# Optimization experiments

Hardware: AMD Instinct MI355X
Metric: run time of the kernel (lower is better)

Reference implementation:

```python
import jax, jax.numpy as jnp
import numpy as np

N_NODES = 20000
N_EDGES = 320000
IN_CH = 256
HID_CH = 256   # 2 * out_channels
OUT_CH = 128


def gcn_conv(x, edge_index, W, b, n_nodes):
    """PyG GCNConv: linear transform, add self-loops, sym-normalized scatter-add."""
    x = x @ W  # [N, C_out]
    loop = jnp.arange(n_nodes, dtype=edge_index.dtype)
    row = jnp.concatenate([edge_index[0], loop])  # source nodes
    col = jnp.concatenate([edge_index[1], loop])  # destination nodes
    deg = jax.ops.segment_sum(jnp.ones_like(col, dtype=x.dtype), col,
                              num_segments=n_nodes)
    deg_inv_sqrt = jnp.where(deg > 0, jax.lax.rsqrt(deg), 0.0)
    norm = deg_inv_sqrt[row] * deg_inv_sqrt[col]  # [E+N]
    msg = x[row] * norm[:, None]                  # gather + scale
    out = jax.ops.segment_sum(msg, col, num_segments=n_nodes)  # scatter-add
    return out + b


def setup_inputs() -> dict:
    key = jax.random.key(0)
    k1, k2, k3, k4, k5 = jax.random.split(key, 5)
    doc_embeds = jax.random.normal(k1, (N_NODES, IN_CH), dtype=jnp.float32)
    edge_index = jax.random.randint(k2, (2, N_EDGES), 0, N_NODES, dtype=jnp.int64)
    # Glorot-style init for GCN weights, zero bias (PyG defaults)
    s1 = 1.0 / np.sqrt(IN_CH)
    s2 = 1.0 / np.sqrt(HID_CH)
    W1 = jax.random.uniform(k3, (IN_CH, HID_CH), jnp.float32, -s1, s1)
    b1 = jnp.zeros((HID_CH,), jnp.float32)
    W2 = jax.random.uniform(k4, (HID_CH, OUT_CH), jnp.float32, -s2, s2)
    b2 = jnp.zeros((OUT_CH,), jnp.float32)
    return {"doc_embeds": doc_embeds, "edge_index": edge_index,
            "W1": W1, "b1": b1, "W2": W2, "b2": b2}


def reference(doc_embeds, edge_index, W1, b1, W2, b2):
    n = doc_embeds.shape[0]
    x = jax.nn.relu(gcn_conv(doc_embeds, edge_index, W1, b1, n))
    x = gcn_conv(x, edge_index, W2, b2, n)
    return x
```

## Files before the change

kernel.cpp:

```cpp
#include <hip/hip_runtime.h>
#include <math.h>

#define N_NODES 20000
#define N_EDGES 320000
#define IN_CH   256
#define HID_CH  256
#define OUT_CH  128
#define CAP     64

typedef __attribute__((ext_vector_type(8))) short short8;
typedef __attribute__((ext_vector_type(8))) unsigned short ushort8;
typedef __attribute__((ext_vector_type(4))) unsigned short ushort4v;
typedef __attribute__((ext_vector_type(4))) float floatx4;
typedef __attribute__((ext_vector_type(2))) float floatx2;
typedef __attribute__((ext_vector_type(4))) _Float16 half4;
typedef __attribute__((ext_vector_type(2))) _Float16 half2v;
typedef __attribute__((ext_vector_type(8))) _Float16 half8;

static __device__ __forceinline__ unsigned short f2bf(float f) {
    unsigned int u = __float_as_uint(f);
    u += 0x7FFFu + ((u >> 16) & 1u);
    return (unsigned short)(u >> 16);
}
static __device__ __forceinline__ float bf2f(unsigned short h) {
    return __uint_as_float(((unsigned int)h) << 16);
}

__global__ __launch_bounds__(256)
void prep_kernel(const float* __restrict__ W1, const float* __restrict__ W2,
                 unsigned short* __restrict__ W1thi, unsigned short* __restrict__ W1tlo,
                 unsigned short* __restrict__ W2thi, unsigned short* __restrict__ W2tlo,
                 const int* __restrict__ row, const int* __restrict__ col,
                 int* __restrict__ deg, unsigned short* __restrict__ srcs) {
    const int g = blockIdx.x * blockDim.x + threadIdx.x;
    const int gsz = gridDim.x * blockDim.x;
    for (int t = g; t < (IN_CH * HID_CH) / 16; t += gsz) {
        int n = t >> 4;
        int kc = (t & 15) * 16;
        ushort8 h0, l0, h1, l1;
#pragma unroll
        for (int j = 0; j < 8; ++j) {
            float x = W1[(size_t)(kc + j) * HID_CH + n];
            h0[j] = f2bf(x); l0[j] = f2bf(x - bf2f(h0[j]));
            float y = W1[(size_t)(kc + 8 + j) * HID_CH + n];
            h1[j] = f2bf(y); l1[j] = f2bf(y - bf2f(h1[j]));
        }
        *(ushort8*)(W1thi + (size_t)n * IN_CH + kc)     = h0;
        *(ushort8*)(W1thi + (size_t)n * IN_CH + kc + 8) = h1;
        *(ushort8*)(W1tlo + (size_t)n * IN_CH + kc)     = l0;
        *(ushort8*)(W1tlo + (size_t)n * IN_CH + kc + 8) = l1;
    }
    for (int t = g; t < (HID_CH * OUT_CH) / 16; t += gsz) {
        int n = t >> 4;
        int kc = (t & 15) * 16;
        ushort8 h0, l0, h1, l1;
#pragma unroll
        for (int j = 0; j < 8; ++j) {
            float x = W2[(size_t)(kc + j) * OUT_CH + n];
            h0[j] = f2bf(x); l0[j] = f2bf(x - bf2f(h0[j]));
            float y = W2[(size_t)(kc + 8 + j) * OUT_CH + n];
            h1[j] = f2bf(y); l1[j] = f2bf(y - bf2f(h1[j]));
        }
        *(ushort8*)(W2thi + (size_t)n * HID_CH + kc)     = h0;
        *(ushort8*)(W2thi + (size_t)n * HID_CH + kc + 8) = h1;
        *(ushort8*)(W2tlo + (size_t)n * HID_CH + kc)     = l0;
        *(ushort8*)(W2tlo + (size_t)n * HID_CH + kc + 8) = l1;
    }
    for (int i = g; i < N_EDGES; i += gsz) {
        int c = col[i];
        int r = row[i];
        int p = atomicAdd(&deg[c], 1);
        srcs[(size_t)c * CAP + p] = (unsigned short)r;
    }
}

#define GK 256
template <int AMODE, int TM>
__global__ __launch_bounds__(256)
void gemm_mfma_kernel(const float* __restrict__ Afp, const _Float16* __restrict__ Ah,
                      const unsigned short* __restrict__ Bthi, const unsigned short* __restrict__ Btlo,
                      const int* __restrict__ deg, _Float16* __restrict__ C, int M, int N) {
    constexpr int MI = TM / 32;
    __shared__ unsigned short As[2][TM][36];
    __shared__ unsigned short Bs[2][128][36];
    const int tid = threadIdx.x;
    const int m0 = blockIdx.y * TM;
    const int n0 = blockIdx.x * 128;
    const int lane = tid & 63;
    const int wave = tid >> 6;
    const int wr = (wave >> 1) * (TM / 2);
    const int wc = (wave & 1) * 64;
    const int lm = lane & 15;
    const int lk = (lane >> 4) * 8;

    floatx4 acc[MI][4];
#pragma unroll
    for (int i = 0; i < MI; ++i)
#pragma unroll
        for (int j = 0; j < 4; ++j) acc[i][j] = (floatx4){0.f, 0.f, 0.f, 0.f};

    for (int k0 = 0; k0 < GK; k0 += 32) {
#pragma unroll
        for (int c = 0; c < TM / 64; ++c) {
            int ch = tid + c * 256;
            int r = ch >> 2;
            int ko = (ch & 3) * 8;
            ushort8 vh = {}, vl = {};
            if (m0 + r < M) {
                float xs[8];
                if (AMODE == 1) {
                    const float* ap = Afp + (size_t)(m0 + r) * GK + k0 + ko;
                    float4 f0 = *(const float4*)ap;
                    float4 f1 = *(const float4*)(ap + 4);
                    xs[0] = f0.x; xs[1] = f0.y; xs[2] = f0.z; xs[3] = f0.w;
                    xs[4] = f1.x; xs[5] = f1.y; xs[6] = f1.z; xs[7] = f1.w;
                } else {
                    half8 hv = *(const half8*)(Ah + (size_t)(m0 + r) * GK + k0 + ko);
#pragma unroll
                    for (int j = 0; j < 8; ++j) xs[j] = (float)hv[j];
                }
#pragma unroll
                for (int j = 0; j < 8; ++j) {
                    vh[j] = f2bf(xs[j]);
                    vl[j] = f2bf(xs[j] - bf2f(vh[j]));
                }
            }
            *(ushort8*)&As[0][r][ko] = vh;
            *(ushort8*)&As[1][r][ko] = vl;
        }
#pragma unroll
        for (int c = 0; c < 2; ++c) {
            int ch = tid + c * 256;
            int r = ch >> 2;
            int ko = (ch & 3) * 8;
            size_t gb = (size_t)(n0 + r) * GK + k0 + ko;
            *(ushort8*)&Bs[0][r][ko] = *(const ushort8*)(Bthi + gb);
            *(ushort8*)&Bs[1][r][ko] = *(const ushort8*)(Btlo + gb);
        }
        __syncthreads();

        short8 ah[MI], al[MI], bh[4], bl[4];
#pragma unroll
        for (int i = 0; i < MI; ++i) {
            ah[i] = *(const short8*)&As[0][wr + i * 16 + lm][lk];
            al[i] = *(const short8*)&As[1][wr + i * 16 + lm][lk];
        }
#pragma unroll
        for (int j = 0; j < 4; ++j) {
            bh[j] = *(const short8*)&Bs[0][wc + j * 16 + lm][lk];
            bl[j] = *(const short8*)&Bs[1][wc + j * 16 + lm][lk];
        }
#pragma unroll
        for (int i = 0; i < MI; ++i)
#pragma unroll
            for (int j = 0; j < 4; ++j) {
                acc[i][j] = __builtin_amdgcn_mfma_f32_16x16x32_bf16(ah[i], bh[j], acc[i][j], 0, 0, 0);
                acc[i][j] = __builtin_amdgcn_mfma_f32_16x16x32_bf16(ah[i], bl[j], acc[i][j], 0, 0, 0);
                acc[i][j] = __builtin_amdgcn_mfma_f32_16x16x32_bf16(al[i], bh[j], acc[i][j], 0, 0, 0);
            }
        __syncthreads();
    }

#pragma unroll
    for (int i = 0; i < MI; ++i) {
#pragma unroll
        for (int r = 0; r < 4; ++r) {
            int rowi = m0 + wr + i * 16 + (lane >> 4) * 4 + r;
            if (rowi < M) {
                float dr = 1.0f / sqrtf((float)(deg[rowi] + 1));
#pragma unroll
                for (int j = 0; j < 4; ++j) {
                    C[(size_t)rowi * N + n0 + wc + j * 16 + lm] = (_Float16)(dr * acc[i][j][r]);
                }
            }
        }
    }
}

template <int C, int NSLICE, int MODE>
__global__ __launch_bounds__(256)
void gather_sliced_kernel(const _Float16* __restrict__ X, const int* __restrict__ deg,
                          const unsigned short* __restrict__ srcs,
                          const float* __restrict__ bias, float* __restrict__ outf,
                          _Float16* __restrict__ outh, int n) {
    constexpr int SW = C / NSLICE;
    static_assert(SW == 32, "slice must be 32 channels");
    const int slice = blockIdx.x % NSLICE;
    const int ngrp  = blockIdx.x / NSLICE;
    const int wave = threadIdx.x >> 6;
    const int lane = threadIdx.x & 63;
    const int g  = lane >> 4;
    const int sl = lane & 15;
    const int node = ngrp * 16 + wave * 4 + g;
    if (node >= n) return;
    const int choff = slice * SW + sl * 2;
    const size_t beg = (size_t)node * CAP;
    const int cnt = deg[node];

    float a0 = 0.f, a1 = 0.f;
    int e = 0;
    for (; e + 4 <= cnt; e += 4) {
        ushort4v s4 = *(const ushort4v*)(srcs + beg + e);
        half2v v0 = *(const half2v*)(X + (size_t)s4.x * C + choff);
        half2v v1 = *(const half2v*)(X + (size_t)s4.y * C + choff);
        half2v v2 = *(const half2v*)(X + (size_t)s4.z * C + choff);
        half2v v3 = *(const half2v*)(X + (size_t)s4.w * C + choff);
        a0 += (float)v0.x + (float)v1.x + (float)v2.x + (float)v3.x;
        a1 += (float)v0.y + (float)v1.y + (float)v2.y + (float)v3.y;
    }
    for (; e < cnt; ++e) {
        int r = srcs[beg + e];
        half2v v = *(const half2v*)(X + (size_t)r * C + choff);
        a0 += (float)v.x; a1 += (float)v.y;
    }

    const float dc = 1.0f / sqrtf((float)(cnt + 1));
    half2v vsh = *(const half2v*)(X + (size_t)node * C + choff);
    float2 bb = *(const float2*)(bias + choff);

    float o0 = dc * (a0 + (float)vsh.x) + bb.x;
    float o1 = dc * (a1 + (float)vsh.y) + bb.y;

    if constexpr (MODE == 1) {
        half2v h;
        h.x = (_Float16)fmaxf(o0, 0.f);
        h.y = (_Float16)fmaxf(o1, 0.f);
        *(half2v*)(outh + (size_t)node * C + choff) = h;
    } else {
        floatx2 o = {o0, o1};
        __builtin_nontemporal_store(o, (floatx2*)(outf + (size_t)node * C + choff));
    }
}

extern "C" void kernel_launch(void* const* d_in, const int* in_sizes, int n_in,
                              void* d_out, int out_size, void* d_ws, size_t ws_size,
                              hipStream_t stream) {
    const float* doc_embeds = (const float*)d_in[0];
    const int*   edge_index = (const int*)d_in[1];
    const float* W1 = (const float*)d_in[2];
    const float* b1 = (const float*)d_in[3];
    const float* W2 = (const float*)d_in[4];
    const float* b2 = (const float*)d_in[5];
    float* out = (float*)d_out;

    const int* row = edge_index;
    const int* col = edge_index + N_EDGES;

    char* ws = (char*)d_ws;
    auto align_up = [](size_t x) { return (x + 255) / 256 * 256; };

    _Float16* X1s = (_Float16*)(ws);
    _Float16* H1  = (_Float16*)(ws + align_up((size_t)N_NODES * HID_CH * 2));
    _Float16* X2s = X1s;
    char* meta = (char*)(ws + 2 * align_up((size_t)N_NODES * HID_CH * 2));
    unsigned short* W1thi = (unsigned short*)(meta); meta += align_up((size_t)IN_CH * HID_CH * 2);
    unsigned short* W1tlo = (unsigned short*)(meta); meta += align_up((size_t)IN_CH * HID_CH * 2);
    unsigned short* W2thi = (unsigned short*)(meta); meta += align_up((size_t)HID_CH * OUT_CH * 2);
    unsigned short* W2tlo = (unsigned short*)(meta); meta += align_up((size_t)HID_CH * OUT_CH * 2);
    int*            deg   = (int*)(meta);            meta += align_up((size_t)N_NODES * 4);
    unsigned short* srcs  = (unsigned short*)(meta);

    hipMemsetAsync(deg, 0, (size_t)N_NODES * 4, stream);
    prep_kernel<<<(N_EDGES + 255) / 256, 256, 0, stream>>>(
        W1, W2, W1thi, W1tlo, W2thi, W2tlo, row, col, deg, srcs);

    {
        dim3 grid(HID_CH / 128, (N_NODES + 63) / 64);
        gemm_mfma_kernel<1, 64><<<grid, 256, 0, stream>>>(
            doc_embeds, nullptr, W1thi, W1tlo, deg, X1s, N_NODES, HID_CH);
    }
    gather_sliced_kernel<HID_CH, 8, 1><<<((N_NODES + 15) / 16) * 8, 256, 0, stream>>>(
        X1s, deg, srcs, b1, nullptr, H1, N_NODES);

    {
        dim3 grid(OUT_CH / 128, (N_NODES + 63) / 64);
        gemm_mfma_kernel<2, 64><<<grid, 256, 0, stream>>>(
            nullptr, H1, W2thi, W2tlo, deg, X2s, N_NODES, OUT_CH);
    }
    gather_sliced_kernel<OUT_CH, 4, 0><<<((N_NODES + 15) / 16) * 4, 256, 0, stream>>>(
        X2s, deg, srcs, b2, out, nullptr, N_NODES);
}
```

Measured before the change: 174.5 us.

## Pre-split GEMM A operands into bf16 hi/lo planes outside the GEMM loop

The fp32 input embeddings are now split into bf16 hi/lo arrays once in the prep kernel, and the first aggregation writes its ReLU output directly as bf16 hi/lo planes instead of fp16. The GEMM then loads its A tiles straight from those planes with no per-tile conversion, so both column blocks of the first GEMM no longer redo the split. The second GEMM switches to a 64-wide N tile, giving two column blocks for more parallelism. The cost is more workspace and extra global traffic to write and re-read the split arrays, and the prep kernel does more work serially ahead of everything else.

```diff
diff --git a/kernel.cpp b/kernel.cpp
--- a/kernel.cpp
+++ b/kernel.cpp
@@ -7,15 +7,15 @@
 #define HID_CH  256
 #define OUT_CH  128
 #define CAP     64
+#define GK      256
 
 typedef __attribute__((ext_vector_type(8))) short short8;
 typedef __attribute__((ext_vector_type(8))) unsigned short ushort8;
 typedef __attribute__((ext_vector_type(4))) unsigned short ushort4v;
+typedef __attribute__((ext_vector_type(2))) unsigned short ushort2v;
 typedef __attribute__((ext_vector_type(4))) float floatx4;
 typedef __attribute__((ext_vector_type(2))) float floatx2;
-typedef __attribute__((ext_vector_type(4))) _Float16 half4;
 typedef __attribute__((ext_vector_type(2))) _Float16 half2v;
-typedef __attribute__((ext_vector_type(8))) _Float16 half8;
 
 static __device__ __forceinline__ unsigned short f2bf(float f) {
     unsigned int u = __float_as_uint(f);
@@ -28,8 +28,10 @@
 
 __global__ __launch_bounds__(256)
 void prep_kernel(const float* __restrict__ W1, const float* __restrict__ W2,
+                 const float* __restrict__ doc,
                  unsigned short* __restrict__ W1thi, unsigned short* __restrict__ W1tlo,
                  unsigned short* __restrict__ W2thi, unsigned short* __restrict__ W2tlo,
+                 unsigned short* __restrict__ Ehi, unsigned short* __restrict__ Elo,
                  const int* __restrict__ row, const int* __restrict__ col,
                  int* __restrict__ deg, unsigned short* __restrict__ srcs) {
     const int g = blockIdx.x * blockDim.x + threadIdx.x;
@@ -66,6 +68,27 @@
         *(ushort8*)(W2tlo + (size_t)n * HID_CH + kc)     = l0;
         *(ushort8*)(W2tlo + (size_t)n * HID_CH + kc + 8) = l1;
     }
+    for (int t = g; t < (N_NODES * IN_CH) / 16; t += gsz) {
+        int node = t >> 4;
+        int kc = (t & 15) * 16;
+        const float* ap = doc + (size_t)node * IN_CH + kc;
+        float4 f0 = *(const float4*)(ap);
+        float4 f1 = *(const float4*)(ap + 4);
+        float4 f2 = *(const float4*)(ap + 8);
+        float4 f3 = *(const float4*)(ap + 12);
+        float xs[16] = {f0.x, f0.y, f0.z, f0.w, f1.x, f1.y, f1.z, f1.w,
+                        f2.x, f2.y, f2.z, f2.w, f3.x, f3.y, f3.z, f3.w};
+        ushort8 h0, l0, h1, l1;
+#pragma unroll
+        for (int j = 0; j < 8; ++j) {
+            h0[j] = f2bf(xs[j]);     l0[j] = f2bf(xs[j] - bf2f(h0[j]));
+            h1[j] = f2bf(xs[8 + j]); l1[j] = f2bf(xs[8 + j] - bf2f(h1[j]));
+        }
+        *(ushort8*)(Ehi + (size_t)node * IN_CH + kc)     = h0;
+        *(ushort8*)(Ehi + (size_t)node * IN_CH + kc + 8) = h1;
+        *(ushort8*)(Elo + (size_t)node * IN_CH + kc)     = l0;
+        *(ushort8*)(Elo + (size_t)node * IN_CH + kc + 8) = l1;
+    }
     for (int i = g; i < N_EDGES; i += gsz) {
         int c = col[i];
         int r = row[i];
@@ -74,64 +97,48 @@
     }
 }
 
-#define GK 256
-template <int AMODE, int TM>
+template <int TN>
 __global__ __launch_bounds__(256)
-void gemm_mfma_kernel(const float* __restrict__ Afp, const _Float16* __restrict__ Ah,
+void gemm_mfma_kernel(const unsigned short* __restrict__ Ahi, const unsigned short* __restrict__ Alo,
                       const unsigned short* __restrict__ Bthi, const unsigned short* __restrict__ Btlo,
                       const int* __restrict__ deg, _Float16* __restrict__ C, int M, int N) {
-    constexpr int MI = TM / 32;
-    __shared__ unsigned short As[2][TM][36];
-    __shared__ unsigned short Bs[2][128][36];
+    constexpr int NJ = TN / 32;
+    __shared__ unsigned short As[2][64][36];
+    __shared__ unsigned short Bs[2][TN][36];
     const int tid = threadIdx.x;
-    const int m0 = blockIdx.y * TM;
-    const int n0 = blockIdx.x * 128;
+    const int m0 = blockIdx.y * 64;
+    const int n0 = blockIdx.x * TN;
     const int lane = tid & 63;
     const int wave = tid >> 6;
-    const int wr = (wave >> 1) * (TM / 2);
-    const int wc = (wave & 1) * 64;
+    const int wr = (wave >> 1) * 32;
+    const int wc = (wave & 1) * (TN / 2);
     const int lm = lane & 15;
     const int lk = (lane >> 4) * 8;
 
-    floatx4 acc[MI][4];
-#pragma unroll
-    for (int i = 0; i < MI; ++i)
-#pragma unroll
-        for (int j = 0; j < 4; ++j) acc[i][j] = (floatx4){0.f, 0.f, 0.f, 0.f};
+    floatx4 acc[2][NJ];
+#pragma unroll
+    for (int i = 0; i < 2; ++i)
+#pragma unroll
+        for (int j = 0; j < NJ; ++j) acc[i][j] = (floatx4){0.f, 0.f, 0.f, 0.f};
+
+    const int ar  = tid >> 2;
+    const int ako = (tid & 3) * 8;
 
     for (int k0 = 0; k0 < GK; k0 += 32) {
-#pragma unroll
-        for (int c = 0; c < TM / 64; ++c) {
+        {
+            ushort8 vh = {}, vl = {};
+            if (m0 + ar < M) {
+                size_t ga = (size_t)(m0 + ar) * GK + k0 + ako;
+                vh = *(const ushort8*)(Ahi + ga);
+                vl = *(const ushort8*)(Alo + ga);
+            }
+            *(ushort8*)&As[0][ar][ako] = vh;
+            *(ushort8*)&As[1][ar][ako] = vl;
+        }
+#pragma unroll
+        for (int c = 0; c < TN / 64; ++c) {
             int ch = tid + c * 256;
-            int r = ch >> 2;
-            int ko = (ch & 3) * 8;
-            ushort8 vh = {}, vl = {};
-            if (m0 + r < M) {
-                float xs[8];
-                if (AMODE == 1) {
-                    const float* ap = Afp + (size_t)(m0 + r) * GK + k0 + ko;
-                    float4 f0 = *(const float4*)ap;
-                    float4 f1 = *(const float4*)(ap + 4);
-                    xs[0] = f0.x; xs[1] = f0.y; xs[2] = f0.z; xs[3] = f0.w;
-                    xs[4] = f1.x; xs[5] = f1.y; xs[6] = f1.z; xs[7] = f1.w;
-                } else {
-                    half8 hv = *(const half8*)(Ah + (size_t)(m0 + r) * GK + k0 + ko);
-#pragma unroll
-                    for (int j = 0; j < 8; ++j) xs[j] = (float)hv[j];
-                }
-#pragma unroll
-                for (int j = 0; j < 8; ++j) {
-                    vh[j] = f2bf(xs[j]);
-                    vl[j] = f2bf(xs[j] - bf2f(vh[j]));
-                }
-            }
-            *(ushort8*)&As[0][r][ko] = vh;
-            *(ushort8*)&As[1][r][ko] = vl;
-        }
-#pragma unroll
-        for (int c = 0; c < 2; ++c) {
-            int ch = tid + c * 256;
-            int r = ch >> 2;
+            int r  = ch >> 2;
             int ko = (ch & 3) * 8;
             size_t gb = (size_t)(n0 + r) * GK + k0 + ko;
             *(ushort8*)&Bs[0][r][ko] = *(const ushort8*)(Bthi + gb);
@@ -139,21 +146,21 @@
         }
         __syncthreads();
 
-        short8 ah[MI], al[MI], bh[4], bl[4];
-#pragma unroll
-        for (int i = 0; i < MI; ++i) {
+        short8 ah[2], al[2], bh[NJ], bl[NJ];
+#pragma unroll
+        for (int i = 0; i < 2; ++i) {
             ah[i] = *(const short8*)&As[0][wr + i * 16 + lm][lk];
             al[i] = *(const short8*)&As[1][wr + i * 16 + lm][lk];
         }
 #pragma unroll
-        for (int j = 0; j < 4; ++j) {
+        for (int j = 0; j < NJ; ++j) {
             bh[j] = *(const short8*)&Bs[0][wc + j * 16 + lm][lk];
             bl[j] = *(const short8*)&Bs[1][wc + j * 16 + lm][lk];
         }
 #pragma unroll
-        for (int i = 0; i < MI; ++i)
-#pragma unroll
-            for (int j = 0; j < 4; ++j) {
+        for (int i = 0; i < 2; ++i)
+#pragma unroll
+            for (int j = 0; j < NJ; ++j) {
                 acc[i][j] = __builtin_amdgcn_mfma_f32_16x16x32_bf16(ah[i], bh[j], acc[i][j], 0, 0, 0);
                 acc[i][j] = __builtin_amdgcn_mfma_f32_16x16x32_bf16(ah[i], bl[j], acc[i][j], 0, 0, 0);
                 acc[i][j] = __builtin_amdgcn_mfma_f32_16x16x32_bf16(al[i], bh[j], acc[i][j], 0, 0, 0);
@@ -162,14 +169,14 @@
     }
 
 #pragma unroll
-    for (int i = 0; i < MI; ++i) {
+    for (int i = 0; i < 2; ++i) {
 #pragma unroll
         for (int r = 0; r < 4; ++r) {
             int rowi = m0 + wr + i * 16 + (lane >> 4) * 4 + r;
             if (rowi < M) {
                 float dr = 1.0f / sqrtf((float)(deg[rowi] + 1));
 #pragma unroll
-                for (int j = 0; j < 4; ++j) {
+                for (int j = 0; j < NJ; ++j) {
                     C[(size_t)rowi * N + n0 + wc + j * 16 + lm] = (_Float16)(dr * acc[i][j][r]);
                 }
             }
@@ -182,7 +189,8 @@
 void gather_sliced_kernel(const _Float16* __restrict__ X, const int* __restrict__ deg,
                           const unsigned short* __restrict__ srcs,
                           const float* __restrict__ bias, float* __restrict__ outf,
-                          _Float16* __restrict__ outh, int n) {
+                          unsigned short* __restrict__ outhi, unsigned short* __restrict__ outlo,
+                          int n) {
     constexpr int SW = C / NSLICE;
     static_assert(SW == 32, "slice must be 32 channels");
     const int slice = blockIdx.x % NSLICE;
@@ -222,10 +230,12 @@
     float o1 = dc * (a1 + (float)vsh.y) + bb.y;
 
     if constexpr (MODE == 1) {
-        half2v h;
-        h.x = (_Float16)fmaxf(o0, 0.f);
-        h.y = (_Float16)fmaxf(o1, 0.f);
-        *(half2v*)(outh + (size_t)node * C + choff) = h;
+        float r0 = fmaxf(o0, 0.f), r1 = fmaxf(o1, 0.f);
+        ushort2v hv, lv;
+        hv.x = f2bf(r0); lv.x = f2bf(r0 - bf2f(hv.x));
+        hv.y = f2bf(r1); lv.y = f2bf(r1 - bf2f(hv.y));
+        *(ushort2v*)(outhi + (size_t)node * C + choff) = hv;
+        *(ushort2v*)(outlo + (size_t)node * C + choff) = lv;
     } else {
         floatx2 o = {o0, o1};
         __builtin_nontemporal_store(o, (floatx2*)(outf + (size_t)node * C + choff));
@@ -247,36 +257,37 @@
     const int* col = edge_index + N_EDGES;
 
     char* ws = (char*)d_ws;
-    auto align_up = [](size_t x) { return (x + 255) / 256 * 256; };
-
-    _Float16* X1s = (_Float16*)(ws);
-    _Float16* H1  = (_Float16*)(ws + align_up((size_t)N_NODES * HID_CH * 2));
-    _Float16* X2s = X1s;
-    char* meta = (char*)(ws + 2 * align_up((size_t)N_NODES * HID_CH * 2));
-    unsigned short* W1thi = (unsigned short*)(meta); meta += align_up((size_t)IN_CH * HID_CH * 2);
-    unsigned short* W1tlo = (unsigned short*)(meta); meta += align_up((size_t)IN_CH * HID_CH * 2);
-    unsigned short* W2thi = (unsigned short*)(meta); meta += align_up((size_t)HID_CH * OUT_CH * 2);
-    unsigned short* W2tlo = (unsigned short*)(meta); meta += align_up((size_t)HID_CH * OUT_CH * 2);
-    int*            deg   = (int*)(meta);            meta += align_up((size_t)N_NODES * 4);
-    unsigned short* srcs  = (unsigned short*)(meta);
+    auto au = [](size_t x) { return (x + 255) / 256 * 256; };
+
+    _Float16* X1s = (_Float16*)ws;      ws += au((size_t)N_NODES * HID_CH * 2);
+    unsigned short* Ehi  = (unsigned short*)ws; ws += au((size_t)N_NODES * IN_CH * 2);
+    unsigned short* Elo  = (unsigned short*)ws; ws += au((size_t)N_NODES * IN_CH * 2);
+    unsigned short* H1hi = (unsigned short*)ws; ws += au((size_t)N_NODES * HID_CH * 2);
+    unsigned short* H1lo = (unsigned short*)ws; ws += au((size_t)N_NODES * HID_CH * 2);
+    unsigned short* W1thi = (unsigned short*)ws; ws += au((size_t)IN_CH * HID_CH * 2);
+    unsigned short* W1tlo = (unsigned short*)ws; ws += au((size_t)IN_CH * HID_CH * 2);
+    unsigned short* W2thi = (unsigned short*)ws; ws += au((size_t)HID_CH * OUT_CH * 2);
+    unsigned short* W2tlo = (unsigned short*)ws; ws += au((size_t)HID_CH * OUT_CH * 2);
+    int*            deg   = (int*)ws;            ws += au((size_t)N_NODES * 4);
+    unsigned short* srcs  = (unsigned short*)ws;
 
     hipMemsetAsync(deg, 0, (size_t)N_NODES * 4, stream);
     prep_kernel<<<(N_EDGES + 255) / 256, 256, 0, stream>>>(
-        W1, W2, W1thi, W1tlo, W2thi, W2tlo, row, col, deg, srcs);
+        W1, W2, doc_embeds, W1thi, W1tlo, W2thi, W2tlo, Ehi, Elo, row, col, deg, srcs);
 
     {
         dim3 grid(HID_CH / 128, (N_NODES + 63) / 64);
-        gemm_mfma_kernel<1, 64><<<grid, 256, 0, stream>>>(
-            doc_embeds, nullptr, W1thi, W1tlo, deg, X1s, N_NODES, HID_CH);
+        gemm_mfma_kernel<128><<<grid, 256, 0, stream>>>(
+            Ehi, Elo, W1thi, W1tlo, deg, X1s, N_NODES, HID_CH);
     }
     gather_sliced_kernel<HID_CH, 8, 1><<<((N_NODES + 15) / 16) * 8, 256, 0, stream>>>(
-        X1s, deg, srcs, b1, nullptr, H1, N_NODES);
+        X1s, deg, srcs, b1, nullptr, H1hi, H1lo, N_NODES);
 
     {
-        dim3 grid(OUT_CH / 128, (N_NODES + 63) / 64);
-        gemm_mfma_kernel<2, 64><<<grid, 256, 0, stream>>>(
-            nullptr, H1, W2thi, W2tlo, deg, X2s, N_NODES, OUT_CH);
+        dim3 grid(OUT_CH / 64, (N_NODES + 63) / 64);
+        gemm_mfma_kernel<64><<<grid, 256, 0, stream>>>(
+            H1hi, H1lo, W2thi, W2tlo, deg, X1s, N_NODES, OUT_CH);
     }
     gather_sliced_kernel<OUT_CH, 4, 0><<<((N_NODES + 15) / 16) * 4, 256, 0, stream>>>(
-        X2s, deg, srcs, b2, out, nullptr, N_NODES);
-}
+        X1s, deg, srcs, b2, out, nullptr, nullptr, N_NODES);
+}
```

New measurement: 181.9 us. +4.2%, slower.
